# Kernel optimization log

Hardware: AMD Instinct MI355X
Metric: run time of the kernel (lower is better)

## Reference

```python
import jax, jax.numpy as jnp
import numpy as np

N = 50000      # nodes
E = 300000     # edges
B = 256        # graphs
F = 128        # feat_dim
F2 = 256       # gnn width = 2*feat_dim
Q = 64         # qubit_num
A = 2016       # action_num
L = 10         # SAGEConv layers
NEG = 0.01     # leaky_relu slope
EPS = 1e-5


def _leaky(v):
    return jnp.where(v > 0, v, NEG * v)


def setup_inputs() -> dict:
    key = jax.random.key(0)
    ks = jax.random.split(key, 16)
    s = 0.05
    x = jax.random.randint(ks[0], (N, 2), 0, Q + 1)
    edge_index = jax.random.randint(ks[1], (2, E), 0, N)
    batch = jnp.sort(jax.random.randint(ks[2], (N,), 0, B))
    emb = (jax.random.normal(ks[3], (Q + 1, F)) * s).at[0].set(0.0)  # padding_idx=0
    Wl = jax.random.normal(ks[4], (L, F2, F2)) * s   # SAGEConv lin_l (neighbor)
    bl = jnp.zeros((L, F2))
    Wr = jax.random.normal(ks[5], (L, F2, F2)) * s   # SAGEConv lin_r (root), no bias
    gn_weight = jnp.ones((F2,))
    gn_bias = jnp.zeros((F2,))
    gn_scale = jnp.ones((F2,))                        # GraphNorm mean_scale
    t = jnp.array(1.0, dtype=jnp.float32)             # SoftmaxAggregation temperature
    W1 = jax.random.normal(ks[6], (F2, F2)) * s
    b1 = jnp.zeros((F2,))
    W2 = jax.random.normal(ks[7], (F2, F)) * s
    b2 = jnp.zeros((F,))
    W3 = jax.random.normal(ks[8], (F, A)) * s
    b3 = jnp.zeros((A,))
    return dict(x=x, edge_index=edge_index, batch=batch, emb=emb, Wl=Wl, bl=bl,
                Wr=Wr, gn_weight=gn_weight, gn_bias=gn_bias, gn_scale=gn_scale,
                t=t, W1=W1, b1=b1, W2=W2, b2=b2, W3=W3, b3=b3)


def reference(x, edge_index, batch, emb, Wl, bl, Wr, gn_weight, gn_bias,
              gn_scale, t, W1, b1, W2, b2, W3, b3):
    # node embedding: two qubit tokens per node -> [N, 2F] = [N, F2]
    h = emb.at[0].set(0.0)[x].reshape(-1, F2)
    src, dst = edge_index[0], edge_index[1]
    deg = jax.ops.segment_sum(jnp.ones((E,), h.dtype), dst, num_segments=N)
    deg = jnp.maximum(deg, 1.0)[:, None]
    for i in range(L):
        agg = jax.ops.segment_sum(h[src], dst, num_segments=N) / deg  # [N, F2]
        h2 = agg @ Wl[i] + bl[i] + h @ Wr[i]
        h = _leaky(h2) + h2
    # GraphNorm (per-graph mean/var with learnable mean_scale)
    cnt = jnp.maximum(jax.ops.segment_sum(jnp.ones((N,), h.dtype), batch,
                                          num_segments=B), 1.0)[:, None]
    mean = jax.ops.segment_sum(h, batch, num_segments=B) / cnt
    o = h - mean[batch] * gn_scale
    var = jax.ops.segment_sum(o * o, batch, num_segments=B) / cnt
    h = gn_weight * o / jnp.sqrt(var + EPS)[batch] + gn_bias
    # SoftmaxAggregation (per-graph, per-channel segment softmax weights)
    logits = h * t
    m = jax.ops.segment_max(logits, batch, num_segments=B)
    ex = jnp.exp(logits - m[batch])
    den = jax.ops.segment_sum(ex, batch, num_segments=B)
    alpha = ex / den[batch]
    g = jax.ops.segment_sum(alpha * h, batch, num_segments=B)  # [B, F2]
    # MLP head
    y = _leaky(g @ W1 + b1)
    y = _leaky(y @ W2 + b2)
    return y @ W3 + b3  # [B, A]
```

## Files before the change

kernel.cpp:

```cpp
#include <hip/hip_runtime.h>

typedef unsigned short u16;
typedef __bf16 bf16x8 __attribute__((ext_vector_type(8)));
typedef float floatx4 __attribute__((ext_vector_type(4)));

#define NN 50000
#define EE 300000
#define BB 256
#define MPAD 50048
#define CAP 32
#define AA 2016

__device__ __forceinline__ float b2f(u16 u) {
    union { float f; unsigned int i; } x; x.i = ((unsigned int)u) << 16; return x.f;
}
__device__ __forceinline__ float lo16(unsigned int w) {
    union { float f; unsigned int i; } x; x.i = w << 16; return x.f;
}
__device__ __forceinline__ float hi16(unsigned int w) {
    union { float f; unsigned int i; } x; x.i = w & 0xffff0000u; return x.f;
}
__device__ __forceinline__ u16 f2b(float f) {
    union { float f; unsigned int i; } x; x.f = f;
    unsigned int r = (x.i + 0x7fffu + ((x.i >> 16) & 1u)) >> 16;
    return (u16)r;
}
__device__ __forceinline__ float loadf(const void* p, size_t i, int md) {
    return md ? ((const float*)p)[i] : b2f(((const u16*)p)[i]);
}

typedef const void __attribute__((address_space(1)))* gas_ptr;
typedef void __attribute__((address_space(3)))* las_ptr;
#define ASYNC_COPY16(gp, lp) \
    __builtin_amdgcn_global_load_lds((gas_ptr)(const void*)(gp), (las_ptr)(void*)(lp), 16, 0, 0)

__global__ void sniff_kernel(const u16* __restrict__ tp, int* __restrict__ mode) {
    *mode = (tp[0] == 0x3F80u) ? 0 : 1;
}

__global__ __launch_bounds__(256) void embed_kernel(const int* __restrict__ x,
                                                    const void* __restrict__ emb,
                                                    const int* __restrict__ mode,
                                                    u16* __restrict__ h) {
    int md = *mode;
    int idx = blockIdx.x * 256 + threadIdx.x;
    int n = idx >> 6, lane = idx & 63;
    int c4 = lane * 4;
    int which = (c4 >> 7) & 1;
    int tok = x[n * 2 + which];
    int ec = c4 & 127;
    size_t ei = (size_t)tok * 128 + ec;
    float e0, e1, e2, e3;
    if (md) {
        float4 v = *(const float4*)((const float*)emb + ei);
        e0 = v.x; e1 = v.y; e2 = v.z; e3 = v.w;
    } else {
        ushort4 v = *(const ushort4*)((const u16*)emb + ei);
        e0 = b2f(v.x); e1 = b2f(v.y); e2 = b2f(v.z); e3 = b2f(v.w);
    }
    ushort4 o;
    o.x = f2b(e0); o.y = f2b(e1); o.z = f2b(e2); o.w = f2b(e3);
    *(ushort4*)&h[(size_t)n * 256 + c4] = o;
}

__global__ __launch_bounds__(256) void scatter_kernel(const int* __restrict__ src,
                                                      const int* __restrict__ dst,
                                                      int* __restrict__ cur,
                                                      int* __restrict__ csrc) {
    int i = blockIdx.x * 256 + threadIdx.x;
    if (i < EE) {
        int d = dst[i];
        int slot = atomicAdd(&cur[d], 1);
        if (slot < CAP) csrc[(size_t)d * CAP + slot] = src[i];
    }
}

__global__ __launch_bounds__(256) void invd_kernel(const int* __restrict__ cur,
                                                   float* __restrict__ invd) {
    int n = blockIdx.x * 256 + threadIdx.x;
    if (n < NN) {
        int d = cur[n];
        invd[n] = 1.0f / (float)(d > 1 ? d : 1);
    }
}

__global__ __launch_bounds__(512) void goff_bs_kernel(const int* __restrict__ batch,
                                                      int* __restrict__ goff) {
    int t = threadIdx.x;
    if (t > BB) return;
    int lo = 0, hi = NN;
    while (lo < hi) {
        int mid = (lo + hi) >> 1;
        if (batch[mid] < t) lo = mid + 1; else hi = mid;
    }
    goff[t] = lo;
}

__global__ __launch_bounds__(256) void transpose_kernel(const void* __restrict__ Wl,
                                                        const void* __restrict__ Wr,
                                                        const int* __restrict__ mode,
                                                        u16* __restrict__ Wt) {
    __shared__ float tile[32][33];
    int md = *mode;
    int w2 = blockIdx.z;
    const void* Ws = (w2 & 1) ? Wr : Wl;
    size_t base = (size_t)(w2 >> 1) * 65536;
    u16* Wo = Wt + (size_t)w2 * 65536;
    int kt = blockIdx.y * 32, nt = blockIdx.x * 32;
    int tx = threadIdx.x, ty = threadIdx.y;
#pragma unroll
    for (int q = 0; q < 4; ++q)
        tile[ty + q * 8][tx] = loadf(Ws, base + (size_t)(kt + ty + q * 8) * 256 + nt + tx, md);
    __syncthreads();
#pragma unroll
    for (int q = 0; q < 4; ++q)
        Wo[(size_t)(nt + ty + q * 8) * 256 + kt + tx] = f2b(tile[tx][ty + q * 8]);
}

__global__ __launch_bounds__(256) void agg_kernel(const u16* __restrict__ h,
                                                  const int* __restrict__ cur,
                                                  const int* __restrict__ csrc,
                                                  const float* __restrict__ invd,
                                                  u16* __restrict__ agg) {
    int node = blockIdx.x * 4 + (threadIdx.x >> 6);
    int lane = threadIdx.x & 63;
    int half = lane >> 5, l32 = lane & 31;
    int cnt = cur[node]; if (cnt > CAP) cnt = CAP;
    const int s = node * CAP;
    float a[8] = {};
    for (int p = s + half; p < s + cnt; p += 2) {
        int sn = csrc[p];
        uint4 hv = *(const uint4*)&h[(size_t)sn * 256 + l32 * 8];
        a[0] += lo16(hv.x); a[1] += hi16(hv.x);
        a[2] += lo16(hv.y); a[3] += hi16(hv.y);
        a[4] += lo16(hv.z); a[5] += hi16(hv.z);
        a[6] += lo16(hv.w); a[7] += hi16(hv.w);
    }
#pragma unroll
    for (int j = 0; j < 8; ++j) a[j] += __shfl_xor(a[j], 32, 64);
    if (half == 0) {
        float id = invd[node];
        u16 o[8];
#pragma unroll
        for (int j = 0; j < 8; ++j) o[j] = f2b(a[j] * id);
        *(uint4*)&agg[(size_t)node * 256 + l32 * 8] = *(uint4*)o;
    }
}

__global__ __launch_bounds__(256) void gemm_kernel(const u16* __restrict__ A0,
                                                   const u16* __restrict__ A1,
                                                   const u16* __restrict__ B0,
                                                   const u16* __restrict__ B1,
                                                   const void* __restrict__ blv,
                                                   int layer,
                                                   const int* __restrict__ mode,
                                                   u16* __restrict__ Hout) {
    __shared__ __align__(16) u16 As[2][128 * 64];
    __shared__ __align__(16) u16 Bs[2][128 * 64];
    int md = *mode;
    const int tid = threadIdx.x;
    const int lane = tid & 63;
    const int wv = tid >> 6;
    const int wm = wv >> 1, wn = wv & 1;
    const int m0 = blockIdx.x * 128;
    const int n0 = blockIdx.y * 128;
    const int r8 = lane >> 3, c8 = lane & 7;
    const int r16 = lane & 15, q = lane >> 4;

    floatx4 acc[4][4] = {};

    auto issue = [&](int kt, int p) {
        const u16* __restrict__ Asrc = (kt < 4) ? A0 : A1;
        const u16* __restrict__ Bsrc = (kt < 4) ? B0 : B1;
        const int koff = (kt & 3) * 64;
#pragma unroll
        for (int j = 0; j < 4; ++j) {
            int row = wv * 32 + j * 8 + r8;
            int cg = c8 ^ (row & 7);
            int ga = m0 + row; if (ga > NN - 1) ga = NN - 1;
            ASYNC_COPY16(Asrc + (size_t)ga * 256 + koff + cg * 8,
                         &As[p][(wv * 32 + j * 8) * 64]);
            ASYNC_COPY16(Bsrc + (size_t)(n0 + row) * 256 + koff + cg * 8,
                         &Bs[p][(wv * 32 + j * 8) * 64]);
        }
    };

    issue(0, 0);
    for (int kt = 0; kt < 8; ++kt) {
        __syncthreads();
        if (kt < 7) issue(kt + 1, (kt + 1) & 1);
        const int p = kt & 1;
#pragma unroll
        for (int ks = 0; ks < 2; ++ks) {
            bf16x8 av[4], bv[4];
            const int swc = ((ks * 4 + q) ^ (lane & 7)) * 8;
#pragma unroll
            for (int mt = 0; mt < 4; ++mt)
                av[mt] = *(const bf16x8*)&As[p][(wm * 64 + mt * 16 + r16) * 64 + swc];
#pragma unroll
            for (int nt = 0; nt < 4; ++nt)
                bv[nt] = *(const bf16x8*)&Bs[p][(wn * 64 + nt * 16 + r16) * 64 + swc];
#pragma unroll
            for (int mt = 0; mt < 4; ++mt)
#pragma unroll
                for (int nt = 0; nt < 4; ++nt)
                    acc[mt][nt] = __builtin_amdgcn_mfma_f32_16x16x32_bf16(
                        bv[nt], av[mt], acc[mt][nt], 0, 0, 0);
        }
    }
#pragma unroll
    for (int nt = 0; nt < 4; ++nt) {
        int gn = n0 + wn * 64 + nt * 16 + q * 4;
        float b0 = loadf(blv, (size_t)layer * 256 + gn + 0, md);
        float b1 = loadf(blv, (size_t)layer * 256 + gn + 1, md);
        float b2 = loadf(blv, (size_t)layer * 256 + gn + 2, md);
        float b3 = loadf(blv, (size_t)layer * 256 + gn + 3, md);
#pragma unroll
        for (int mt = 0; mt < 4; ++mt) {
            int gm = m0 + wm * 64 + mt * 16 + r16;
            if (gm < NN) {
                float v0 = acc[mt][nt][0] + b0;
                float v1 = acc[mt][nt][1] + b1;
                float v2 = acc[mt][nt][2] + b2;
                float v3 = acc[mt][nt][3] + b3;
                v0 = (v0 > 0.f) ? 2.f * v0 : 1.01f * v0;
                v1 = (v1 > 0.f) ? 2.f * v1 : 1.01f * v1;
                v2 = (v2 > 0.f) ? 2.f * v2 : 1.01f * v2;
                v3 = (v3 > 0.f) ? 2.f * v3 : 1.01f * v3;
                ushort4 o;
                o.x = f2b(v0); o.y = f2b(v1); o.z = f2b(v2); o.w = f2b(v3);
                *(ushort4*)&Hout[(size_t)gm * 256 + gn] = o;
            }
        }
    }
}

__global__ __launch_bounds__(1024) void gn_softmax_kernel(const u16* __restrict__ h,
                                                          const int* __restrict__ goff,
                                                          const void* __restrict__ gnw,
                                                          const void* __restrict__ gnb,
                                                          const void* __restrict__ gns,
                                                          const void* __restrict__ tp,
                                                          const int* __restrict__ mode,
                                                          float* __restrict__ g) {
    __shared__ float red[1024];
    __shared__ float red2[1024];
    int md = *mode;
    const int sub = threadIdx.x >> 8;
    const int c = threadIdx.x & 255;
    const int b = blockIdx.x;
    const int s = goff[b], e = goff[b + 1];
    const int cn = e - s;
    const float icnt = 1.0f / (float)(cn > 1 ? cn : 1);

    float sum = 0.f, sq = 0.f;
#pragma unroll 4
    for (int n = s + sub; n < e; n += 4) {
        float hv = b2f(h[(size_t)n * 256 + c]);
        sum += hv; sq += hv * hv;
    }
    red[threadIdx.x] = sum; red2[threadIdx.x] = sq; __syncthreads();
    float mean = (red[c] + red[256 + c] + red[512 + c] + red[768 + c]) * icnt;
    float e2 = (red2[c] + red2[256 + c] + red2[512 + c] + red2[768 + c]) * icnt;
    float msc = mean * loadf(gns, c, md);
    float var = e2 - 2.f * msc * mean + msc * msc;
    if (var < 0.f) var = 0.f;
    float w = loadf(gnw, c, md) * rsqrtf(var + 1e-5f);
    float bb = loadf(gnb, c, md);
    float tv = loadf(tp, 0, md);
    __syncthreads();

    float den = 0.f, num = 0.f;
#pragma unroll 4
    for (int n = s + sub; n < e; n += 4) {
        float hn = w * (b2f(h[(size_t)n * 256 + c]) - msc) + bb;
        float elv = __expf(fminf(hn * tv, 60.f));
        den += elv; num += elv * hn;
    }
    red[threadIdx.x] = den; red2[threadIdx.x] = num; __syncthreads();
    if (sub == 0) {
        float D = red[c] + red[256 + c] + red[512 + c] + red[768 + c];
        float Nu = red2[c] + red2[256 + c] + red2[512 + c] + red2[768 + c];
        g[b * 256 + c] = (D > 1e-30f) ? (Nu / D) : 0.f;
    }
}

__global__ __launch_bounds__(256) void y1_kernel(const float* __restrict__ g,
                                                 const void* __restrict__ W1,
                                                 const void* __restrict__ b1,
                                                 const int* __restrict__ mode,
                                                 float* __restrict__ y1) {
    __shared__ float gr[256];
    int md = *mode;
    int row = blockIdx.x, t = threadIdx.x;
    gr[t] = g[row * 256 + t];
    __syncthreads();
    float acc = 0.f;
    if (md) {
        const float* W = (const float*)W1;
#pragma unroll 8
        for (int k = 0; k < 256; ++k) acc += gr[k] * W[(size_t)k * 256 + t];
    } else {
        const u16* W = (const u16*)W1;
#pragma unroll 8
        for (int k = 0; k < 256; ++k) acc += gr[k] * b2f(W[(size_t)k * 256 + t]);
    }
    float v = acc + loadf(b1, t, md);
    y1[row * 256 + t] = (v > 0.f) ? v : 0.01f * v;
}

__global__ __launch_bounds__(128) void y2_kernel(const float* __restrict__ y1,
                                                 const void* __restrict__ W2,
                                                 const void* __restrict__ b2v,
                                                 const int* __restrict__ mode,
                                                 float* __restrict__ y2) {
    __shared__ float yr[256];
    int md = *mode;
    int row = blockIdx.x, t = threadIdx.x;
    yr[t] = y1[row * 256 + t];
    yr[t + 128] = y1[row * 256 + t + 128];
    __syncthreads();
    float acc = 0.f;
    if (md) {
        const float* W = (const float*)W2;
#pragma unroll 8
        for (int k = 0; k < 256; ++k) acc += yr[k] * W[(size_t)k * 128 + t];
    } else {
        const u16* W = (const u16*)W2;
#pragma unroll 8
        for (int k = 0; k < 256; ++k) acc += yr[k] * b2f(W[(size_t)k * 128 + t]);
    }
    float v = acc + loadf(b2v, t, md);
    y2[row * 128 + t] = (v > 0.f) ? v : 0.01f * v;
}

__global__ __launch_bounds__(256) void out_kernel(const float* __restrict__ y2,
                                                  const void* __restrict__ W3,
                                                  const void* __restrict__ b3,
                                                  const int* __restrict__ mode,
                                                  void* __restrict__ outp) {
    __shared__ float yr[128];
    int md = *mode;
    int row = blockIdx.y;
    int col = blockIdx.x * 256 + threadIdx.x;
    if (threadIdx.x < 128) yr[threadIdx.x] = y2[row * 128 + threadIdx.x];
    __syncthreads();
    if (col >= AA) return;
    float acc = 0.f;
    if (md) {
        const float* W = (const float*)W3;
#pragma unroll 8
        for (int k = 0; k < 128; ++k) acc += yr[k] * W[(size_t)k * AA + col];
    } else {
        const u16* W = (const u16*)W3;
#pragma unroll 8
        for (int k = 0; k < 128; ++k) acc += yr[k] * b2f(W[(size_t)k * AA + col]);
    }
    float v = acc + loadf(b3, col, md);
    if (md) ((float*)outp)[(size_t)row * AA + col] = v;
    else    ((u16*)outp)[(size_t)row * AA + col] = f2b(v);
}

extern "C" void kernel_launch(void* const* d_in, const int* in_sizes, int n_in,
                              void* d_out, int out_size, void* d_ws, size_t ws_size,
                              hipStream_t stream) {
    const int* xi    = (const int*)d_in[0];
    const int* ei    = (const int*)d_in[1];
    const int* srcp  = ei;
    const int* dstp  = ei + EE;
    const int* batch = (const int*)d_in[2];
    const void* emb = d_in[3];
    const void* Wl  = d_in[4];
    const void* bl  = d_in[5];
    const void* Wr  = d_in[6];
    const void* gnw = d_in[7];
    const void* gnb = d_in[8];
    const void* gns = d_in[9];
    const void* tp  = d_in[10];
    const void* W1  = d_in[11];
    const void* b1  = d_in[12];
    const void* W2  = d_in[13];
    const void* b2v = d_in[14];
    const void* W3  = d_in[15];
    const void* b3  = d_in[16];

    unsigned char* ws = (unsigned char*)d_ws;
    size_t off = 0;
    auto alloc = [&](size_t b) -> size_t {
        size_t o = off; off = (off + b + 255) & ~(size_t)255; return o;
    };
    size_t hA_o  = alloc((size_t)MPAD * 256 * 2);
    size_t hB_o  = alloc((size_t)MPAD * 256 * 2);
    size_t agg_o = alloc((size_t)MPAD * 256 * 2);
    size_t Wt_o  = alloc((size_t)20 * 65536 * 2);
    size_t cur_o = alloc((size_t)NN * 4);
    size_t csrc_o = alloc((size_t)NN * CAP * 4);
    size_t invd_o = alloc((size_t)NN * 4);
    size_t goff_o = alloc((size_t)(BB + 1) * 4);
    size_t g_o   = alloc((size_t)BB * 256 * 4);
    size_t y1_o  = alloc((size_t)BB * 256 * 4);
    size_t y2_o  = alloc((size_t)BB * 128 * 4);
    size_t mode_o = alloc(256);

    u16* hA   = (u16*)(ws + hA_o);
    u16* hB   = (u16*)(ws + hB_o);
    u16* aggb = (u16*)(ws + agg_o);
    u16* Wt   = (u16*)(ws + Wt_o);
    int* cur  = (int*)(ws + cur_o);
    int* csrc = (int*)(ws + csrc_o);
    float* invd = (float*)(ws + invd_o);
    int* goff = (int*)(ws + goff_o);
    float* gbuf = (float*)(ws + g_o);
    float* y1b  = (float*)(ws + y1_o);
    float* y2b  = (float*)(ws + y2_o);
    int* modep  = (int*)(ws + mode_o);

    hipMemsetAsync(ws + cur_o, 0, (size_t)NN * 4, stream);

    sniff_kernel<<<1, 1, 0, stream>>>((const u16*)tp, modep);
    embed_kernel<<<12500, 256, 0, stream>>>(xi, emb, modep, hA);
    transpose_kernel<<<dim3(8, 8, 20), dim3(32, 8), 0, stream>>>(Wl, Wr, modep, Wt);
    scatter_kernel<<<(EE + 255) / 256, 256, 0, stream>>>(srcp, dstp, cur, csrc);
    invd_kernel<<<(NN + 255) / 256, 256, 0, stream>>>(cur, invd);
    goff_bs_kernel<<<1, 512, 0, stream>>>(batch, goff);

    u16* hcur = hA;
    u16* hnxt = hB;
    for (int l = 0; l < 10; ++l) {
        agg_kernel<<<12500, 256, 0, stream>>>(hcur, cur, csrc, invd, aggb);
        gemm_kernel<<<dim3(391, 2), 256, 0, stream>>>(
            aggb, hcur,
            Wt + (size_t)(2 * l) * 65536, Wt + (size_t)(2 * l + 1) * 65536,
            bl, l, modep, hnxt);
        u16* t2 = hcur; hcur = hnxt; hnxt = t2;
    }

    gn_softmax_kernel<<<BB, 1024, 0, stream>>>(hcur, goff, gnw, gnb, gns, tp, modep, gbuf);
    y1_kernel<<<BB, 256, 0, stream>>>(gbuf, W1, b1, modep, y1b);
    y2_kernel<<<BB, 128, 0, stream>>>(y1b, W2, b2v, modep, y2b);
    out_kernel<<<dim3(8, BB), 256, 0, stream>>>(y2b, W3, b3, modep, d_out);
}
```

Before: 820.7 us.

## Load GEMM weights directly from global, halve LDS, and merge setup kernels

```diff
diff --git a/kernel.cpp b/kernel.cpp
--- a/kernel.cpp
+++ b/kernel.cpp
@@ -34,16 +34,14 @@
 #define ASYNC_COPY16(gp, lp) \
     __builtin_amdgcn_global_load_lds((gas_ptr)(const void*)(gp), (las_ptr)(void*)(lp), 16, 0, 0)
 
-__global__ void sniff_kernel(const u16* __restrict__ tp, int* __restrict__ mode) {
-    *mode = (tp[0] == 0x3F80u) ? 0 : 1;
-}
-
 __global__ __launch_bounds__(256) void embed_kernel(const int* __restrict__ x,
                                                     const void* __restrict__ emb,
                                                     const int* __restrict__ mode,
-                                                    u16* __restrict__ h) {
+                                                    u16* __restrict__ h,
+                                                    int* __restrict__ cur) {
     int md = *mode;
     int idx = blockIdx.x * 256 + threadIdx.x;
+    if (idx < NN) cur[idx] = 0;
     int n = idx >> 6, lane = idx & 63;
     int c4 = lane * 4;
     int which = (c4 >> 7) & 1;
@@ -85,8 +83,11 @@
 }
 
 __global__ __launch_bounds__(512) void goff_bs_kernel(const int* __restrict__ batch,
-                                                      int* __restrict__ goff) {
+                                                      const u16* __restrict__ tp,
+                                                      int* __restrict__ goff,
+                                                      int* __restrict__ mode) {
     int t = threadIdx.x;
+    if (t == 511) *mode = (tp[0] == 0x3F80u) ? 0 : 1;
     if (t > BB) return;
     int lo = 0, hi = NN;
     while (lo < hi) {
@@ -147,16 +148,15 @@
     }
 }
 
-__global__ __launch_bounds__(256) void gemm_kernel(const u16* __restrict__ A0,
-                                                   const u16* __restrict__ A1,
-                                                   const u16* __restrict__ B0,
-                                                   const u16* __restrict__ B1,
-                                                   const void* __restrict__ blv,
-                                                   int layer,
-                                                   const int* __restrict__ mode,
-                                                   u16* __restrict__ Hout) {
+__global__ __launch_bounds__(256, 3) void gemm_kernel(const u16* __restrict__ A0,
+                                                      const u16* __restrict__ A1,
+                                                      const u16* __restrict__ B0,
+                                                      const u16* __restrict__ B1,
+                                                      const void* __restrict__ blv,
+                                                      int layer,
+                                                      const int* __restrict__ mode,
+                                                      u16* __restrict__ Hout) {
     __shared__ __align__(16) u16 As[2][128 * 64];
-    __shared__ __align__(16) u16 Bs[2][128 * 64];
     int md = *mode;
     const int tid = threadIdx.x;
     const int lane = tid & 63;
@@ -169,9 +169,8 @@
 
     floatx4 acc[4][4] = {};
 
-    auto issue = [&](int kt, int p) {
+    auto issueA = [&](int kt, int p) {
         const u16* __restrict__ Asrc = (kt < 4) ? A0 : A1;
-        const u16* __restrict__ Bsrc = (kt < 4) ? B0 : B1;
         const int koff = (kt & 3) * 64;
 #pragma unroll
         for (int j = 0; j < 4; ++j) {
@@ -180,32 +179,36 @@
             int ga = m0 + row; if (ga > NN - 1) ga = NN - 1;
             ASYNC_COPY16(Asrc + (size_t)ga * 256 + koff + cg * 8,
                          &As[p][(wv * 32 + j * 8) * 64]);
-            ASYNC_COPY16(Bsrc + (size_t)(n0 + row) * 256 + koff + cg * 8,
-                         &Bs[p][(wv * 32 + j * 8) * 64]);
         }
     };
 
-    issue(0, 0);
+    issueA(0, 0);
     for (int kt = 0; kt < 8; ++kt) {
         __syncthreads();
-        if (kt < 7) issue(kt + 1, (kt + 1) & 1);
+        if (kt < 7) issueA(kt + 1, (kt + 1) & 1);
+        const u16* __restrict__ Bsrc = (kt < 4) ? B0 : B1;
+        const int koff = (kt & 3) * 64;
         const int p = kt & 1;
+        bf16x8 bv[2][4];
+#pragma unroll
+        for (int ks = 0; ks < 2; ++ks)
+#pragma unroll
+            for (int nt = 0; nt < 4; ++nt)
+                bv[ks][nt] = *(const bf16x8*)&Bsrc[(size_t)(n0 + wn * 64 + nt * 16 + r16) * 256
+                                                   + koff + (ks * 4 + q) * 8];
 #pragma unroll
         for (int ks = 0; ks < 2; ++ks) {
-            bf16x8 av[4], bv[4];
+            bf16x8 av[4];
             const int swc = ((ks * 4 + q) ^ (lane & 7)) * 8;
 #pragma unroll
             for (int mt = 0; mt < 4; ++mt)
                 av[mt] = *(const bf16x8*)&As[p][(wm * 64 + mt * 16 + r16) * 64 + swc];
 #pragma unroll
-            for (int nt = 0; nt < 4; ++nt)
-                bv[nt] = *(const bf16x8*)&Bs[p][(wn * 64 + nt * 16 + r16) * 64 + swc];
-#pragma unroll
             for (int mt = 0; mt < 4; ++mt)
 #pragma unroll
                 for (int nt = 0; nt < 4; ++nt)
                     acc[mt][nt] = __builtin_amdgcn_mfma_f32_16x16x32_bf16(
-                        bv[nt], av[mt], acc[mt][nt], 0, 0, 0);
+                        bv[ks][nt], av[mt], acc[mt][nt], 0, 0, 0);
         }
     }
 #pragma unroll
@@ -415,14 +418,11 @@
     float* y2b  = (float*)(ws + y2_o);
     int* modep  = (int*)(ws + mode_o);
 
-    hipMemsetAsync(ws + cur_o, 0, (size_t)NN * 4, stream);
-
-    sniff_kernel<<<1, 1, 0, stream>>>((const u16*)tp, modep);
-    embed_kernel<<<12500, 256, 0, stream>>>(xi, emb, modep, hA);
+    goff_bs_kernel<<<1, 512, 0, stream>>>(batch, (const u16*)tp, goff, modep);
+    embed_kernel<<<12500, 256, 0, stream>>>(xi, emb, modep, hA, cur);
     transpose_kernel<<<dim3(8, 8, 20), dim3(32, 8), 0, stream>>>(Wl, Wr, modep, Wt);
     scatter_kernel<<<(EE + 255) / 256, 256, 0, stream>>>(srcp, dstp, cur, csrc);
     invd_kernel<<<(NN + 255) / 256, 256, 0, stream>>>(cur, invd);
-    goff_bs_kernel<<<1, 512, 0, stream>>>(batch, goff);
 
     u16* hcur = hA;
     u16* hnxt = hB;
```

Measured after the change: 966.7 us. +17.8%, slower.
